# Kernel optimization log

Hardware: AMD Instinct MI355X
Metric: run time of the kernel (lower is better)

## Reference

```python
import jax, jax.numpy as jnp
import numpy as np

GAMMA = 1.05  # VoxelSampler.GAMMA


def setup_inputs() -> dict:
    key = jax.random.key(0)
    k1, k2, k3, k4, k5 = jax.random.split(key, 5)
    B, T, R, Np, F = 2, 8, 128, 32768, 5
    # point xy within pc_range, remaining features (z, intensity, ...) gaussian
    xy = jax.random.uniform(k1, (B, T, Np, 2), minval=-75.0, maxval=75.0)
    rest = jax.random.normal(k2, (B, T, Np, F - 2))
    points = jnp.concatenate([xy, rest], axis=-1)  # [B,T,Np,5]
    # rois: [cx,cy,cz, dx,dy,dz, yaw, vx,vy]
    ctr = jax.random.uniform(k3, (B, T, R, 3), minval=-75.0, maxval=75.0)
    dims = jax.random.uniform(k4, (B, T, R, 3), minval=1.0, maxval=6.0)
    yaw_vel = jax.random.normal(k5, (B, T, R, 3))
    trajectory_rois = jnp.concatenate([ctr, dims, yaw_vel], axis=-1)  # [B,T,R,9]
    return {"points": points, "trajectory_rois": trajectory_rois, "num_sample": 32}


def reference(points, trajectory_rois, num_sample):
    # points: [B,T,Np,5] (pre-partitioned per batch/frame, mirrors the
    # batch-column + timestamp masking of the torch code with static shapes)
    # trajectory_rois: [B,T,R,9]
    B, T, R, _ = trajectory_rois.shape
    Fdim = points.shape[-1]
    # speed = ||roi[..., -2:]||, per-roi gamma = clamp((1.05*(1+speed))**(t/5), max=2.5)
    speed = jnp.linalg.norm(trajectory_rois[..., 7:9], axis=-1)          # [B,T,R]
    t_idx = jnp.arange(T, dtype=points.dtype)
    gamma = jnp.minimum((GAMMA * (1.0 + speed)) ** (t_idx[None, :, None] / 5.0), 2.5)
    # cylindrical radius per roi: ||dims_xy/2|| * gamma
    radiis = jnp.linalg.norm(trajectory_rois[..., 3:5] * 0.5, axis=-1) * gamma  # [B,T,R]
    cx = trajectory_rois[..., 0]
    cy = trajectory_rois[..., 1]
    px = points[..., 0]
    py = points[..., 1]
    dx = px[:, :, None, :] - cx[..., None]   # [B,T,R,Np]
    dy = py[:, :, None, :] - cy[..., None]
    dis = jnp.sqrt(dx * dx + dy * dy)        # [B,T,R,Np]
    in_radius = (dis <= radiis[..., None]).astype(points.dtype)
    # topk over 0/1 mask: picks num_sample in-radius points (lowest indices first),
    # exactly like torch.topk(point_mask.float(), num_sample)
    vals, idx = jax.lax.top_k(in_radius, num_sample)  # [B,T,R,S]
    sampled = jnp.take_along_axis(points[:, :, None, :, :], idx[..., None], axis=3)  # [B,T,R,S,5]
    sampled = jnp.where(vals[..., None] > 0, sampled, jnp.zeros((), dtype=points.dtype))
    # stack frames -> permute(0,2,1,3,4) -> flatten(2,3): [B,R,T*S,5]
    out = jnp.transpose(sampled, (0, 2, 1, 3, 4)).reshape(B, R, T * num_sample, Fdim)
    return out
```

## Files before the change

### kernel.cpp

```cpp
#include <hip/hip_runtime.h>
#include <math.h>

#define B_   2
#define T_   8
#define R_   128
#define NP_  32768
#define F_   5
#define S_   32
#define SEG_ 2048
#define NSEG (NP_ / SEG_)
#define NBT  (B_ * T_)
#define NROW (NBT * R_)
#define RPB  8

__device__ __forceinline__ int mbcnt64(unsigned long long m) {
    return __builtin_amdgcn_mbcnt_hi((unsigned)(m >> 32),
           __builtin_amdgcn_mbcnt_lo((unsigned)m, 0u));
}

__global__ __launch_bounds__(256) void xy_transpose_prep(
    const float* __restrict__ points,
    const float* __restrict__ rois,
    float2* __restrict__ xy,
    float4* __restrict__ rowc)
{
    const int j = blockIdx.x * blockDim.x + threadIdx.x;
    if (j < NBT * NP_ / 4) {
        const float4* src = (const float4*)points + (size_t)j * 5;
        const float4 a = src[0], b = src[1], c = src[2], d = src[3], e = src[4];
        float4* dst = (float4*)xy + (size_t)j * 2;
        dst[0] = make_float4(a.x, a.y, b.y, b.z);
        dst[1] = make_float4(c.z, c.w, d.w, e.x);
    }
    if (j < NROW) {
        const int row = j;
        const int bt  = row / R_;
        const int t   = bt % T_;
        const float* roi = rois + (size_t)row * 9;
        const float cx = roi[0], cy = roi[1];
        const float hx = roi[3] * 0.5f, hy = roi[4] * 0.5f;
        const float vx = roi[7], vy = roi[8];
        const float speed  = sqrtf(vx * vx + vy * vy);
        const float base_g = 1.05f * (1.0f + speed);
        const float expo   = (float)t / 5.0f;
        const float gamma  = fminf((float)pow((double)base_g, (double)expo), 2.5f);
        const float radius = sqrtf(hx * hx + hy * hy) * gamma;
        unsigned ut = __float_as_uint(radius * radius);
        while (sqrtf(__uint_as_float(ut)) > radius) --ut;
        while (sqrtf(__uint_as_float(ut + 1u)) <= radius) ++ut;
        rowc[row] = make_float4(cx, cy, __uint_as_float(ut), 0.0f);
    }
}

__global__ __launch_bounds__(256) void phase1_collect(
    const float2* __restrict__ xy,
    const float4* __restrict__ rowc,
    int* __restrict__ counts,
    unsigned short* __restrict__ hitidx)
{
    __shared__ float4 tile[SEG_ / 2];

    const int blk = blockIdx.x;
    const int rg  = blk % (R_ / RPB);
    const int bs  = blk / (R_ / RPB);
    const int seg = bs % NSEG;
    const int bt  = bs / NSEG;
    const int w    = threadIdx.x >> 6;
    const int lane = threadIdx.x & 63;

    const float4* src = (const float4*)(xy + (size_t)bt * NP_ + (size_t)seg * SEG_);
    #pragma unroll
    for (int i = 0; i < 4; ++i)
        tile[i * 256 + threadIdx.x] = src[i * 256 + threadIdx.x];
    __syncthreads();

    const int row0 = bt * R_ + rg * RPB + w * 2;
    const int row1 = row0 + 1;
    const float4 rc0 = rowc[row0], rc1 = rowc[row1];
    unsigned short* h0 = hitidx + ((size_t)row0 * NSEG + seg) * S_;
    unsigned short* h1 = hitidx + ((size_t)row1 * NSEG + seg) * S_;

    int sel0 = 0, sel1 = 0;
    const int ibase = seg * SEG_;
    #pragma unroll 2
    for (int it = 0; it < SEG_ / 128; ++it) {
        const float4 q = tile[it * 64 + lane];
        const int idx0 = ibase + (it * 64 + lane) * 2;

        {
            const float ax = __fsub_rn(q.x, rc0.x), ay = __fsub_rn(q.y, rc0.y);
            const float bx = __fsub_rn(q.z, rc0.x), by = __fsub_rn(q.w, rc0.y);
            const float d2a = __fadd_rn(__fmul_rn(ax, ax), __fmul_rn(ay, ay));
            const float d2b = __fadd_rn(__fmul_rn(bx, bx), __fmul_rn(by, by));
            const bool p0 = (d2a <= rc0.z), p1 = (d2b <= rc0.z);
            const unsigned long long m0 = __ballot(p0), m1 = __ballot(p1);
            if (m0 | m1) {
                const int base = sel0 + mbcnt64(m0) + mbcnt64(m1);
                if (p0 && base < S_) h0[base] = (unsigned short)idx0;
                if (p1) { const int s = base + (p0 ? 1 : 0);
                          if (s < S_) h0[s] = (unsigned short)(idx0 + 1); }
                sel0 += __popcll(m0) + __popcll(m1);
            }
        }
        {
            const float ax = __fsub_rn(q.x, rc1.x), ay = __fsub_rn(q.y, rc1.y);
            const float bx = __fsub_rn(q.z, rc1.x), by = __fsub_rn(q.w, rc1.y);
            const float d2a = __fadd_rn(__fmul_rn(ax, ax), __fmul_rn(ay, ay));
            const float d2b = __fadd_rn(__fmul_rn(bx, bx), __fmul_rn(by, by));
            const bool p0 = (d2a <= rc1.z), p1 = (d2b <= rc1.z);
            const unsigned long long m0 = __ballot(p0), m1 = __ballot(p1);
            if (m0 | m1) {
                const int base = sel1 + mbcnt64(m0) + mbcnt64(m1);
                if (p0 && base < S_) h1[base] = (unsigned short)idx0;
                if (p1) { const int s = base + (p0 ? 1 : 0);
                          if (s < S_) h1[s] = (unsigned short)(idx0 + 1); }
                sel1 += __popcll(m0) + __popcll(m1);
            }
        }
    }
    if (lane == 0) {
        counts[(size_t)row0 * NSEG + seg] = (sel0 < S_) ? sel0 : S_;
        counts[(size_t)row1 * NSEG + seg] = (sel1 < S_) ? sel1 : S_;
    }
}

__global__ __launch_bounds__(256) void phase2_gather(
    const float* __restrict__ points,
    const int* __restrict__ counts,
    const unsigned short* __restrict__ hitidx,
    float* __restrict__ out)
{
    const int tid  = blockIdx.x * blockDim.x + threadIdx.x;
    const int slot = tid & (S_ - 1);
    const int row  = tid >> 5;
    if (row >= NROW) return;
    const int r  = row % R_;
    const int bt = row / R_;
    const int t  = bt % T_;
    const int b  = bt / T_;

    const int4* cp = (const int4*)(counts + (size_t)row * NSEG);
    const int4 q0 = cp[0], q1 = cp[1], q2 = cp[2], q3 = cp[3];
    const int cs[16] = {q0.x,q0.y,q0.z,q0.w, q1.x,q1.y,q1.z,q1.w,
                        q2.x,q2.y,q2.z,q2.w, q3.x,q3.y,q3.z,q3.w};
    int seg = -1, local = 0, acc = 0;
    #pragma unroll
    for (int s = 0; s < NSEG; ++s) {
        const int na = acc + cs[s];
        if (seg < 0 && slot < na) { seg = s; local = slot - acc; }
        acc = na;
    }
    const int total = (acc < S_) ? acc : S_;

    float* o = out + (((((size_t)b * R_ + r) * T_ + t) * S_) + slot) * F_;
    if (slot < total) {
        const int pi = hitidx[((size_t)row * NSEG + seg) * S_ + local];
        const float* p = points + ((size_t)bt * NP_ + pi) * F_;
        o[0] = p[0]; o[1] = p[1]; o[2] = p[2]; o[3] = p[3]; o[4] = p[4];
    } else {
        o[0] = 0.0f; o[1] = 0.0f; o[2] = 0.0f; o[3] = 0.0f; o[4] = 0.0f;
    }
}

extern "C" void kernel_launch(void* const* d_in, const int* in_sizes, int n_in,
                              void* d_out, int out_size, void* d_ws, size_t ws_size,
                              hipStream_t stream) {
    const float* points = (const float*)d_in[0];
    const float* rois   = (const float*)d_in[1];
    float* out = (float*)d_out;

    char* ws = (char*)d_ws;
    float2* xy             = (float2*)ws;
    int* counts            = (int*)(ws + 4194304);
    unsigned short* hitidx = (unsigned short*)(ws + 4194304 + 131072);
    float4* rowc           = (float4*)(ws + 4194304 + 131072 + 2097152);

    xy_transpose_prep<<<(NBT * NP_ / 4 + 255) / 256, 256, 0, stream>>>(points, rois, xy, rowc);

    phase1_collect<<<NBT * NSEG * (R_ / RPB), 256, 0, stream>>>(xy, rowc, counts, hitidx);

    phase2_gather<<<(NROW * S_) / 256, 256, 0, stream>>>(points, counts, hitidx, out);
}
```

Measured before the change: 84.41 us.

## Fuse xy transpose and roi prep into the collect kernel

Removes the separate prep kernel that wrote a compact xy array and per-row circle constants to workspace. The collect kernel now reads the raw 5-float points for its segment straight into shared memory, extracting xy on the fly. Lanes 0 and 1 of each wave compute their row's center and squared-radius threshold, and the values are broadcast with shuffles. This saves one launch and the xy round trip through memory. In exchange, each block rereads the full 20-byte points instead of 8-byte xy, and the roi threshold math (double pow) is redone in every block.

```diff
diff --git a/kernel.cpp b/kernel.cpp
--- a/kernel.cpp
+++ b/kernel.cpp
@@ -18,23 +18,38 @@
            __builtin_amdgcn_mbcnt_lo((unsigned)m, 0u));
 }
 
-__global__ __launch_bounds__(256) void xy_transpose_prep(
+__global__ __launch_bounds__(256) void phase1_collect(
     const float* __restrict__ points,
     const float* __restrict__ rois,
-    float2* __restrict__ xy,
-    float4* __restrict__ rowc)
+    int* __restrict__ counts,
+    unsigned short* __restrict__ hitidx)
 {
-    const int j = blockIdx.x * blockDim.x + threadIdx.x;
-    if (j < NBT * NP_ / 4) {
-        const float4* src = (const float4*)points + (size_t)j * 5;
-        const float4 a = src[0], b = src[1], c = src[2], d = src[3], e = src[4];
-        float4* dst = (float4*)xy + (size_t)j * 2;
-        dst[0] = make_float4(a.x, a.y, b.y, b.z);
-        dst[1] = make_float4(c.z, c.w, d.w, e.x);
+    __shared__ float4 tile[SEG_ / 2];
+
+    const int blk = blockIdx.x;
+    const int rg  = blk % (R_ / RPB);
+    const int bs  = blk / (R_ / RPB);
+    const int seg = bs % NSEG;
+    const int bt  = bs / NSEG;
+    const int tid  = threadIdx.x;
+    const int w    = tid >> 6;
+    const int lane = tid & 63;
+
+    const float4* src = (const float4*)(points + (size_t)bt * NP_ * F_)
+                        + (size_t)seg * (SEG_ * F_ / 4);
+    #pragma unroll
+    for (int i = 0; i < 2; ++i) {
+        const int g = tid + i * 256;
+        const float4* s5 = src + (size_t)g * 5;
+        const float4 a = s5[0], bq = s5[1], c = s5[2], d = s5[3], e = s5[4];
+        tile[g * 2]     = make_float4(a.x, a.y, bq.y, bq.z);
+        tile[g * 2 + 1] = make_float4(c.z, c.w, d.w, e.x);
     }
-    if (j < NROW) {
-        const int row = j;
-        const int bt  = row / R_;
+
+    const int row0 = bt * R_ + rg * RPB + w * 2;
+    float vcx = 0.0f, vcy = 0.0f, vT = 0.0f;
+    if (lane < 2) {
+        const int row = row0 + lane;
         const int t   = bt % T_;
         const float* roi = rois + (size_t)row * 9;
         const float cx = roi[0], cy = roi[1];
@@ -48,35 +63,14 @@
         unsigned ut = __float_as_uint(radius * radius);
         while (sqrtf(__uint_as_float(ut)) > radius) --ut;
         while (sqrtf(__uint_as_float(ut + 1u)) <= radius) ++ut;
-        rowc[row] = make_float4(cx, cy, __uint_as_float(ut), 0.0f);
+        vcx = cx; vcy = cy; vT = __uint_as_float(ut);
     }
-}
+    const float cx0 = __shfl(vcx, 0), cy0 = __shfl(vcy, 0), T0 = __shfl(vT, 0);
+    const float cx1 = __shfl(vcx, 1), cy1 = __shfl(vcy, 1), T1 = __shfl(vT, 1);
 
-__global__ __launch_bounds__(256) void phase1_collect(
-    const float2* __restrict__ xy,
-    const float4* __restrict__ rowc,
-    int* __restrict__ counts,
-    unsigned short* __restrict__ hitidx)
-{
-    __shared__ float4 tile[SEG_ / 2];
-
-    const int blk = blockIdx.x;
-    const int rg  = blk % (R_ / RPB);
-    const int bs  = blk / (R_ / RPB);
-    const int seg = bs % NSEG;
-    const int bt  = bs / NSEG;
-    const int w    = threadIdx.x >> 6;
-    const int lane = threadIdx.x & 63;
-
-    const float4* src = (const float4*)(xy + (size_t)bt * NP_ + (size_t)seg * SEG_);
-    #pragma unroll
-    for (int i = 0; i < 4; ++i)
-        tile[i * 256 + threadIdx.x] = src[i * 256 + threadIdx.x];
     __syncthreads();
 
-    const int row0 = bt * R_ + rg * RPB + w * 2;
     const int row1 = row0 + 1;
-    const float4 rc0 = rowc[row0], rc1 = rowc[row1];
     unsigned short* h0 = hitidx + ((size_t)row0 * NSEG + seg) * S_;
     unsigned short* h1 = hitidx + ((size_t)row1 * NSEG + seg) * S_;
 
@@ -88,11 +82,11 @@
         const int idx0 = ibase + (it * 64 + lane) * 2;
 
         {
-            const float ax = __fsub_rn(q.x, rc0.x), ay = __fsub_rn(q.y, rc0.y);
-            const float bx = __fsub_rn(q.z, rc0.x), by = __fsub_rn(q.w, rc0.y);
+            const float ax = __fsub_rn(q.x, cx0), ay = __fsub_rn(q.y, cy0);
+            const float bx = __fsub_rn(q.z, cx0), by = __fsub_rn(q.w, cy0);
             const float d2a = __fadd_rn(__fmul_rn(ax, ax), __fmul_rn(ay, ay));
             const float d2b = __fadd_rn(__fmul_rn(bx, bx), __fmul_rn(by, by));
-            const bool p0 = (d2a <= rc0.z), p1 = (d2b <= rc0.z);
+            const bool p0 = (d2a <= T0), p1 = (d2b <= T0);
             const unsigned long long m0 = __ballot(p0), m1 = __ballot(p1);
             if (m0 | m1) {
                 const int base = sel0 + mbcnt64(m0) + mbcnt64(m1);
@@ -103,11 +97,11 @@
             }
         }
         {
-            const float ax = __fsub_rn(q.x, rc1.x), ay = __fsub_rn(q.y, rc1.y);
-            const float bx = __fsub_rn(q.z, rc1.x), by = __fsub_rn(q.w, rc1.y);
+            const float ax = __fsub_rn(q.x, cx1), ay = __fsub_rn(q.y, cy1);
+            const float bx = __fsub_rn(q.z, cx1), by = __fsub_rn(q.w, cy1);
             const float d2a = __fadd_rn(__fmul_rn(ax, ax), __fmul_rn(ay, ay));
             const float d2b = __fadd_rn(__fmul_rn(bx, bx), __fmul_rn(by, by));
-            const bool p0 = (d2a <= rc1.z), p1 = (d2b <= rc1.z);
+            const bool p0 = (d2a <= T1), p1 = (d2b <= T1);
             const unsigned long long m0 = __ballot(p0), m1 = __ballot(p1);
             if (m0 | m1) {
                 const int base = sel1 + mbcnt64(m0) + mbcnt64(m1);
@@ -170,14 +164,10 @@
     float* out = (float*)d_out;
 
     char* ws = (char*)d_ws;
-    float2* xy             = (float2*)ws;
-    int* counts            = (int*)(ws + 4194304);
-    unsigned short* hitidx = (unsigned short*)(ws + 4194304 + 131072);
-    float4* rowc           = (float4*)(ws + 4194304 + 131072 + 2097152);
+    int* counts            = (int*)ws;
+    unsigned short* hitidx = (unsigned short*)(ws + 131072);
 
-    xy_transpose_prep<<<(NBT * NP_ / 4 + 255) / 256, 256, 0, stream>>>(points, rois, xy, rowc);
-
-    phase1_collect<<<NBT * NSEG * (R_ / RPB), 256, 0, stream>>>(xy, rowc, counts, hitidx);
+    phase1_collect<<<NBT * NSEG * (R_ / RPB), 256, 0, stream>>>(points, rois, counts, hitidx);
 
     phase2_gather<<<(NROW * S_) / 256, 256, 0, stream>>>(points, counts, hitidx, out);
 }
```

Measured after the change: 88.38 us. 4.7% more time.
